# Kernel optimization log

Measured on AMD Instinct MI355X. Metric: run time of the kernel, lower is better.

The kernel has to match this reference:

```python
import jax, jax.numpy as jnp
from jax import lax
import numpy as np

KSIZE = 3  # dynamic depthwise kernel size
DN = ('NCHW', 'OIHW', 'NCHW')


def setup_inputs() -> dict:
    key = jax.random.key(0)
    ks = jax.random.split(key, 6)
    B, C, H, W = 16, 64, 192, 192
    x = jax.random.normal(ks[0], (B, C, H, W), dtype=jnp.float32)
    k_v = jax.random.normal(ks[1], (B, 64), dtype=jnp.float32)
    # kernel-generating MLP (torch nn.Linear weights, y = x @ W.T), scaled for stability
    W1 = jax.random.normal(ks[2], (64, 64), dtype=jnp.float32) * (1.0 / np.sqrt(64))
    W2 = jax.random.normal(ks[3], (C * KSIZE * KSIZE, 64), dtype=jnp.float32) * (1.0 / np.sqrt(64))
    # static Conv2d(C, C, 3, padding=1)
    conv_w = jax.random.normal(ks[4], (C, C, 3, 3), dtype=jnp.float32) * (1.0 / np.sqrt(C * 9))
    conv_b = jax.random.normal(ks[5], (C,), dtype=jnp.float32) * 0.01
    return {"x": x, "k_v": k_v, "W1": W1, "W2": W2, "conv_w": conv_w, "conv_b": conv_b}


def reference(x, k_v, W1, W2, conv_w, conv_b):
    b, c, h, w = x.shape
    pad = (KSIZE - 1) // 2
    # kernel = Linear -> LeakyReLU(0.1) -> Linear, viewed as (b*c, 1, k, k)
    hid = jax.nn.leaky_relu(k_v @ W1.T, negative_slope=0.1)            # (b, 64)
    kern = (hid @ W2.T).reshape(b * c, 1, KSIZE, KSIZE)                # (b*c, 1, k, k)
    # grouped depthwise conv: one distinct kxk kernel per (batch, channel)
    out = lax.conv_general_dilated(
        x.reshape(1, b * c, h, w), kern,
        window_strides=(1, 1), padding=[(pad, pad), (pad, pad)],
        feature_group_count=b * c, dimension_numbers=DN)
    out = jax.nn.leaky_relu(out, negative_slope=0.1).reshape(b, c, h, w)
    # static 3x3 conv residual branch
    res = lax.conv_general_dilated(
        x, conv_w, window_strides=(1, 1), padding=[(1, 1), (1, 1)],
        dimension_numbers=DN) + conv_b[None, :, None, None]
    return out + res
```

## Files before the change

### kernel.cpp

```cpp
#include <hip/hip_runtime.h>

#define B_ 16
#define C_ 64
#define H_ 192
#define W_ 192
#define TR 4
#define TC 48

typedef short bf16x8 __attribute__((ext_vector_type(8)));
typedef float f32x4  __attribute__((ext_vector_type(4)));

static __device__ __forceinline__ unsigned short f2bf(float f) {
    union { float f; unsigned u; } v; v.f = f;
    unsigned r = v.u + 0x7fff + ((v.u >> 16) & 1);
    return (unsigned short)(r >> 16);
}
static __device__ __forceinline__ float bf2f(unsigned short u) {
    union { unsigned u; float f; } v; v.u = ((unsigned)u) << 16; return v.f;
}
static __device__ __forceinline__ int xsw(int p, int ch) {
    return p * 64 + (((ch >> 3) ^ (p & 7)) << 3) + (ch & 7);
}

__global__ void kgen1(const float* __restrict__ k_v, const float* __restrict__ W1,
                      float* __restrict__ hid) {
    int b = blockIdx.x, c = threadIdx.x;
    __shared__ float kv[64];
    kv[c] = k_v[b * 64 + c];
    __syncthreads();
    float s = 0.f;
#pragma unroll
    for (int k = 0; k < 64; ++k) s += kv[k] * W1[c * 64 + k];
    hid[b * 64 + c] = s > 0.f ? s : 0.1f * s;
}

__global__ void kgen2(const float* __restrict__ hid, const float* __restrict__ W2,
                      float* __restrict__ kern) {
    int idx = blockIdx.x * 256 + threadIdx.x;
    int b = idx / 576, o = idx - b * 576;
    const float* h = hid + b * 64;
    const float* w = W2 + o * 64;
    float t = 0.f;
#pragma unroll
    for (int k = 0; k < 64; ++k) t += h[k] * w[k];
    kern[idx] = t;
}

__global__ void wtrans(const float* __restrict__ conv_w, unsigned short* __restrict__ wT) {
    int idx = blockIdx.x * 256 + threadIdx.x;
    int tap = idx >> 12;
    int rem = idx & 4095;
    int n = rem >> 6, k = rem & 63;
    wT[idx] = f2bf(conv_w[(n * 64 + k) * 9 + tap]);
}

__global__ __launch_bounds__(256, 3)
void fused_conv(const float* __restrict__ x, const unsigned short* __restrict__ wT,
                const float* __restrict__ kern, const float* __restrict__ conv_b,
                float* __restrict__ out) {
    const int bx = blockIdx.x;
    const int by = blockIdx.y;
    const int b  = blockIdx.z;
    const int tid  = threadIdx.x;
    const int lane = tid & 63;
    const int wv   = tid >> 6;
    const int n0   = lane & 15;
    const int q    = lane >> 4;
    const int r0 = by * TR;
    const int c0 = bx * TC;

    __shared__ __align__(16) unsigned short xs[6 * 50 * 64];

    for (int u = tid; u < 576; u += 256) {
        int chg  = u / 72;
        int rest = u - chg * 72;
        int row  = rest / 12;
        int cg   = rest - row * 12;
        int gr   = r0 + row - 1;
        bool in  = (gr >= 0 && gr < H_);
        int grc  = in ? gr : 0;
        const float* xp = x + ((size_t)(b * 64 + chg * 8) * H_ + grc) * W_ + c0 + cg * 4;
        float4 f[8];
#pragma unroll
        for (int j = 0; j < 8; ++j)
            f[j] = in ? *(const float4*)(xp + j * H_ * W_) : make_float4(0.f, 0.f, 0.f, 0.f);
#pragma unroll
        for (int e = 0; e < 4; ++e) {
            int p = row * 50 + 1 + cg * 4 + e;
            union { bf16x8 v; unsigned short s[8]; } wv8;
#pragma unroll
            for (int j = 0; j < 8; ++j) wv8.s[j] = f2bf(((const float*)&f[j])[e]);
            *(bf16x8*)(xs + xsw(p, chg * 8)) = wv8.v;
        }
    }
    if (tid < 96) {
        int chg  = tid / 12;
        int rest = tid - chg * 12;
        int row  = rest >> 1;
        int sc   = (rest & 1) ? 49 : 0;
        int gr = r0 + row - 1, gc = c0 + sc - 1;
        bool in = (gr >= 0 && gr < H_ && gc >= 0 && gc < W_);
        union { bf16x8 v; unsigned short s[8]; } wv8;
#pragma unroll
        for (int j = 0; j < 8; ++j) {
            float vv = 0.f;
            if (in) vv = x[((size_t)(b * 64 + chg * 8 + j) * H_ + gr) * W_ + gc];
            wv8.s[j] = f2bf(vv);
        }
        *(bf16x8*)(xs + xsw(row * 50 + sc, chg * 8)) = wv8.v;
    }

    f32x4 acc[3][4];
#pragma unroll
    for (int i = 0; i < 3; ++i)
#pragma unroll
        for (int j = 0; j < 4; ++j) acc[i][j] = (f32x4){0.f, 0.f, 0.f, 0.f};

    __syncthreads();

#pragma unroll
    for (int tap = 0; tap < 9; ++tap) {
        const int dr = tap / 3, dc = tap % 3;
        bf16x8 bf[4][2];
#pragma unroll
        for (int nt = 0; nt < 4; ++nt)
#pragma unroll
            for (int ks = 0; ks < 2; ++ks)
                bf[nt][ks] = *(const bf16x8*)(wT + tap * 4096 + (nt * 16 + n0) * 64 + ks * 32 + q * 8);
#pragma unroll
        for (int cb = 0; cb < 3; ++cb) {
            const int p = (wv + dr) * 50 + cb * 16 + n0 + dc;
            bf16x8 a0 = *(const bf16x8*)(xs + p * 64 + ((q ^ (p & 7)) << 3));
            bf16x8 a1 = *(const bf16x8*)(xs + p * 64 + (((q + 4) ^ (p & 7)) << 3));
#pragma unroll
            for (int nt = 0; nt < 4; ++nt) {
                acc[cb][nt] = __builtin_amdgcn_mfma_f32_16x16x32_bf16(a0, bf[nt][0], acc[cb][nt], 0, 0, 0);
                acc[cb][nt] = __builtin_amdgcn_mfma_f32_16x16x32_bf16(a1, bf[nt][1], acc[cb][nt], 0, 0, 0);
            }
        }
    }

    const float* kp = kern + b * 576;
#pragma unroll
    for (int nt = 0; nt < 4; ++nt) {
        const int n = nt * 16 + n0;
        float kw[9];
#pragma unroll
        for (int j = 0; j < 9; ++j) kw[j] = kp[n * 9 + j];
        const float bias = conv_b[n];
        const int gn = n >> 3, n7 = n & 7;
#pragma unroll
        for (int cb = 0; cb < 3; ++cb) {
            const int colb = cb * 16 + q * 4;
            float xw[3][6];
#pragma unroll
            for (int d = 0; d < 3; ++d)
#pragma unroll
                for (int cc = 0; cc < 6; ++cc) {
                    int p = (wv + d) * 50 + colb + cc;
                    xw[d][cc] = bf2f(xs[p * 64 + ((gn ^ (p & 7)) << 3) + n7]);
                }
            float4 st;
#pragma unroll
            for (int r = 0; r < 4; ++r) {
                float dw = 0.f;
#pragma unroll
                for (int d = 0; d < 3; ++d)
#pragma unroll
                    for (int e = 0; e < 3; ++e)
                        dw += kw[d * 3 + e] * xw[d][r + e];
                float v = (dw > 0.f ? dw : 0.1f * dw) + acc[cb][nt][r] + bias;
                ((float*)&st)[r] = v;
            }
            *(float4*)(out + ((size_t)(b * 64 + n) * H_ + (r0 + wv)) * W_ + c0 + colb) = st;
        }
    }
}

extern "C" void kernel_launch(void* const* d_in, const int* in_sizes, int n_in,
                              void* d_out, int out_size, void* d_ws, size_t ws_size,
                              hipStream_t stream) {
    const float* x      = (const float*)d_in[0];
    const float* k_v    = (const float*)d_in[1];
    const float* W1     = (const float*)d_in[2];
    const float* W2     = (const float*)d_in[3];
    const float* conv_w = (const float*)d_in[4];
    const float* conv_b = (const float*)d_in[5];
    float* outp = (float*)d_out;

    float* kern        = (float*)d_ws;
    unsigned short* wT = (unsigned short*)((char*)d_ws + 40960);
    float* hid         = (float*)((char*)d_ws + 114688);

    kgen1<<<16, 64, 0, stream>>>(k_v, W1, hid);
    kgen2<<<36, 256, 0, stream>>>(hid, W2, kern);
    wtrans<<<144, 256, 0, stream>>>(conv_w, wT);
    dim3 grid(4, 48, 16);
    fused_conv<<<grid, 256, 0, stream>>>(x, wT, kern, conv_b, outp);
}
```

Baseline: 418.0 us.

## Merge prep kernels, remap blocks across XCDs, and prefetch weight fragments per tap

The three small setup kernels (two MLP layers and the weight transpose) become a single prep launch, which removes two launches and the intermediate hidden-vector round trip. The main conv kernel remaps its linear block index so that the eight XCD groups each take a contiguous pair of batches, which is meant to improve L2 locality. The weight B-fragments for the next tap are now loaded one tap ahead, with the first load issued before the shared-memory staging, so global load latency overlaps the MFMAs. This costs extra registers and could reduce occupancy under the 3-blocks launch bound.

Result: faster. 406.1 us (-2.9%).

```diff
diff --git a/kernel.cpp b/kernel.cpp
--- a/kernel.cpp
+++ b/kernel.cpp
@@ -22,45 +22,50 @@
     return p * 64 + (((ch >> 3) ^ (p & 7)) << 3) + (ch & 7);
 }
 
-__global__ void kgen1(const float* __restrict__ k_v, const float* __restrict__ W1,
-                      float* __restrict__ hid) {
-    int b = blockIdx.x, c = threadIdx.x;
-    __shared__ float kv[64];
-    kv[c] = k_v[b * 64 + c];
-    __syncthreads();
-    float s = 0.f;
-#pragma unroll
-    for (int k = 0; k < 64; ++k) s += kv[k] * W1[c * 64 + k];
-    hid[b * 64 + c] = s > 0.f ? s : 0.1f * s;
-}
-
-__global__ void kgen2(const float* __restrict__ hid, const float* __restrict__ W2,
-                      float* __restrict__ kern) {
-    int idx = blockIdx.x * 256 + threadIdx.x;
-    int b = idx / 576, o = idx - b * 576;
-    const float* h = hid + b * 64;
-    const float* w = W2 + o * 64;
-    float t = 0.f;
-#pragma unroll
-    for (int k = 0; k < 64; ++k) t += h[k] * w[k];
-    kern[idx] = t;
-}
-
-__global__ void wtrans(const float* __restrict__ conv_w, unsigned short* __restrict__ wT) {
-    int idx = blockIdx.x * 256 + threadIdx.x;
-    int tap = idx >> 12;
-    int rem = idx & 4095;
-    int n = rem >> 6, k = rem & 63;
-    wT[idx] = f2bf(conv_w[(n * 64 + k) * 9 + tap]);
+__global__ void prep(const float* __restrict__ k_v, const float* __restrict__ W1,
+                     const float* __restrict__ W2, const float* __restrict__ conv_w,
+                     float* __restrict__ kern, unsigned short* __restrict__ wT) {
+    const int blk = blockIdx.x, tid = threadIdx.x;
+    if (blk < 16) {
+        __shared__ float kv[64], hid[64];
+        const int b = blk;
+        if (tid < 64) kv[tid] = k_v[b * 64 + tid];
+        __syncthreads();
+        if (tid < 64) {
+            float s = 0.f;
+#pragma unroll
+            for (int k = 0; k < 64; ++k) s += kv[k] * W1[tid * 64 + k];
+            hid[tid] = s > 0.f ? s : 0.1f * s;
+        }
+        __syncthreads();
+        for (int o = tid; o < 576; o += 256) {
+            const float* w = W2 + o * 64;
+            float t = 0.f;
+#pragma unroll
+            for (int k = 0; k < 64; ++k) t += hid[k] * w[k];
+            kern[b * 576 + o] = t;
+        }
+    } else {
+        int idx = (blk - 16) * 256 + tid;
+        int tap = idx >> 12;
+        int rem = idx & 4095;
+        int n = rem >> 6, k = rem & 63;
+        wT[idx] = f2bf(conv_w[(n * 64 + k) * 9 + tap]);
+    }
 }
 
 __global__ __launch_bounds__(256, 3)
 void fused_conv(const float* __restrict__ x, const unsigned short* __restrict__ wT,
                 const float* __restrict__ kern, const float* __restrict__ conv_b,
                 float* __restrict__ out) {
-    const int bx = blockIdx.x;
-    const int by = blockIdx.y;
-    const int b  = blockIdx.z;
+    const int L = blockIdx.x + 4 * (blockIdx.y + 48 * blockIdx.z);
+    const int g = L & 7;
+    const int s = L >> 3;
+    const int bx = s & 3;
+    const int sl = s >> 2;
+    const int by = sl % 48;
+    const int b  = (g << 1) + (sl / 48);
+
     const int tid  = threadIdx.x;
     const int lane = tid & 63;
     const int wv   = tid >> 6;
@@ -70,6 +75,14 @@
     const int c0 = bx * TC;
 
     __shared__ __align__(16) unsigned short xs[6 * 50 * 64];
+
+    const unsigned short* wbase = wT + n0 * 64 + q * 8;
+    bf16x8 bcur[4][2], bnxt[4][2];
+#pragma unroll
+    for (int nt = 0; nt < 4; ++nt)
+#pragma unroll
+        for (int ks = 0; ks < 2; ++ks)
+            bcur[nt][ks] = *(const bf16x8*)(wbase + nt * 1024 + ks * 32);
 
     for (int u = tid; u < 576; u += 256) {
         int chg  = u / 72;
@@ -87,10 +100,10 @@
 #pragma unroll
         for (int e = 0; e < 4; ++e) {
             int p = row * 50 + 1 + cg * 4 + e;
-            union { bf16x8 v; unsigned short s[8]; } wv8;
-#pragma unroll
-            for (int j = 0; j < 8; ++j) wv8.s[j] = f2bf(((const float*)&f[j])[e]);
-            *(bf16x8*)(xs + xsw(p, chg * 8)) = wv8.v;
+            union { bf16x8 v; unsigned short s8[8]; } pk;
+#pragma unroll
+            for (int j = 0; j < 8; ++j) pk.s8[j] = f2bf(((const float*)&f[j])[e]);
+            *(bf16x8*)(xs + xsw(p, chg * 8)) = pk.v;
         }
     }
     if (tid < 96) {
@@ -100,14 +113,14 @@
         int sc   = (rest & 1) ? 49 : 0;
         int gr = r0 + row - 1, gc = c0 + sc - 1;
         bool in = (gr >= 0 && gr < H_ && gc >= 0 && gc < W_);
-        union { bf16x8 v; unsigned short s[8]; } wv8;
+        union { bf16x8 v; unsigned short s8[8]; } pk;
 #pragma unroll
         for (int j = 0; j < 8; ++j) {
             float vv = 0.f;
             if (in) vv = x[((size_t)(b * 64 + chg * 8 + j) * H_ + gr) * W_ + gc];
-            wv8.s[j] = f2bf(vv);
-        }
-        *(bf16x8*)(xs + xsw(row * 50 + sc, chg * 8)) = wv8.v;
+            pk.s8[j] = f2bf(vv);
+        }
+        *(bf16x8*)(xs + xsw(row * 50 + sc, chg * 8)) = pk.v;
     }
 
     f32x4 acc[3][4];
@@ -120,13 +133,14 @@
 
 #pragma unroll
     for (int tap = 0; tap < 9; ++tap) {
+        if (tap < 8) {
+#pragma unroll
+            for (int nt = 0; nt < 4; ++nt)
+#pragma unroll
+                for (int ks = 0; ks < 2; ++ks)
+                    bnxt[nt][ks] = *(const bf16x8*)(wbase + (tap + 1) * 4096 + nt * 1024 + ks * 32);
+        }
         const int dr = tap / 3, dc = tap % 3;
-        bf16x8 bf[4][2];
-#pragma unroll
-        for (int nt = 0; nt < 4; ++nt)
-#pragma unroll
-            for (int ks = 0; ks < 2; ++ks)
-                bf[nt][ks] = *(const bf16x8*)(wT + tap * 4096 + (nt * 16 + n0) * 64 + ks * 32 + q * 8);
 #pragma unroll
         for (int cb = 0; cb < 3; ++cb) {
             const int p = (wv + dr) * 50 + cb * 16 + n0 + dc;
@@ -134,9 +148,16 @@
             bf16x8 a1 = *(const bf16x8*)(xs + p * 64 + (((q + 4) ^ (p & 7)) << 3));
 #pragma unroll
             for (int nt = 0; nt < 4; ++nt) {
-                acc[cb][nt] = __builtin_amdgcn_mfma_f32_16x16x32_bf16(a0, bf[nt][0], acc[cb][nt], 0, 0, 0);
-                acc[cb][nt] = __builtin_amdgcn_mfma_f32_16x16x32_bf16(a1, bf[nt][1], acc[cb][nt], 0, 0, 0);
+                acc[cb][nt] = __builtin_amdgcn_mfma_f32_16x16x32_bf16(a0, bcur[nt][0], acc[cb][nt], 0, 0, 0);
+                acc[cb][nt] = __builtin_amdgcn_mfma_f32_16x16x32_bf16(a1, bcur[nt][1], acc[cb][nt], 0, 0, 0);
             }
+        }
+        if (tap < 8) {
+#pragma unroll
+            for (int nt = 0; nt < 4; ++nt)
+#pragma unroll
+                for (int ks = 0; ks < 2; ++ks)
+                    bcur[nt][ks] = bnxt[nt][ks];
         }
     }
 
@@ -190,11 +211,8 @@
 
     float* kern        = (float*)d_ws;
     unsigned short* wT = (unsigned short*)((char*)d_ws + 40960);
-    float* hid         = (float*)((char*)d_ws + 114688);
-
-    kgen1<<<16, 64, 0, stream>>>(k_v, W1, hid);
-    kgen2<<<36, 256, 0, stream>>>(hid, W2, kern);
-    wtrans<<<144, 256, 0, stream>>>(conv_w, wT);
+
+    prep<<<160, 256, 0, stream>>>(k_v, W1, W2, conv_w, kern, wT);
     dim3 grid(4, 48, 16);
     fused_conv<<<grid, 256, 0, stream>>>(x, wT, kern, conv_b, outp);
 }
```
